# Kernel tuning notes

Hardware: AMD Instinct MI355X
Metric: run time of the kernel (lower is better)

## Reference

```python
import jax, jax.numpy as jnp
import numpy as np

B, N, M, Q, H, D = 1, 512, 512, 128, 8, 16
CLIP = 10.0

def _xavier(key, shape):
    # xavier_uniform over last two dims (fan_in=Q, fan_out=D per head)
    fan_in, fan_out = shape[-2], shape[-1]
    limit = float(np.sqrt(6.0 / (fan_in + fan_out)))
    return jax.random.uniform(key, shape, jnp.float32, -limit, limit)

def setup_inputs() -> dict:
    key = jax.random.key(0)
    ks = jax.random.split(key, 12)
    return {
        "x": jax.random.normal(ks[0], (B, N, Q), jnp.float32),
        "y": jax.random.normal(ks[1], (B, M, Q), jnp.float32),
        "z": jax.random.normal(ks[2], (B, N, M, Q), jnp.float32),
        "mask": jax.random.randint(ks[3], (B, N, M), 0, 2, jnp.int32),
        "lambda_x": _xavier(ks[4], (H, Q, D)),
        "lambda_y": _xavier(ks[5], (H, Q, D)),
        "lambda_z1": _xavier(ks[6], (H, Q, D)),
        "lambda_z2": _xavier(ks[7], (H, Q, D)),
        "bias_lambda_x": jnp.zeros((H, D), jnp.float32),
        "bias_lambda_y": jnp.zeros((H, D), jnp.float32),
        "theta1": _xavier(ks[8], (H, Q, D)),
        "theta2": _xavier(ks[9], (H, Q, D)),
        "bias_theta": jnp.zeros((H, D), jnp.float32),
    }

def reference(x, y, z, mask, lambda_x, lambda_y, lambda_z1, lambda_z2,
              bias_lambda_x, bias_lambda_y, theta1, theta2, bias_theta):
    head_dim = lambda_x.shape[-1]
    # node projections: [B,N,H,D] / [B,M,H,D]
    r_x = jnp.einsum('bnq,hqd->bnhd', x, lambda_x) + bias_lambda_x
    r_y = jnp.einsum('bmq,hqd->bmhd', y, lambda_y) + bias_lambda_y
    # edge projections: [B,N,M,H,D]
    r_z1 = jnp.einsum('bnmq,hqd->bnmhd', z, lambda_z1)
    r_z2 = jnp.einsum('bnmq,hqd->bnmhd', z, lambda_z2)
    # broadcast-add node + edge terms, dot over D -> scores [B,H,N,M]
    att = jnp.einsum('bnmhd,bnmhd->bhnm',
                     r_x[:, :, None, :, :] + r_z1,
                     r_y[:, None, :, :, :] + r_z2)
    att = att * (head_dim ** -0.5)
    att = CLIP * jnp.tanh(att)
    att = jnp.where(mask[:, None, :, :] == 1, -jnp.inf, att)
    # NOTE: softmax over the N (source) axis, matching torch dim=-2
    w = jax.nn.softmax(att, axis=-2)
    x_p = jnp.einsum('bnq,hqd->bnhd', x, theta1)
    r = jnp.einsum('bhnm,bnhd->bmhd', w, x_p) + bias_theta
    return jnp.einsum('bmhd,hqd->bmq', r, theta2)
```

## Files before the change

kernel.cpp:

```cpp
#include <hip/hip_runtime.h>
#include <hip/hip_bf16.h>
#include <math.h>

typedef __attribute__((ext_vector_type(8))) short short8;
typedef __attribute__((ext_vector_type(4))) float f32x4;

__global__ void pack_kernel(const float* __restrict__ lz1,
                            const float* __restrict__ lz2,
                            const float* __restrict__ th2,
                            const float* __restrict__ bth,
                            const float* __restrict__ lx,
                            const float* __restrict__ ly,
                            const float* __restrict__ t1,
                            __hip_bfloat16* __restrict__ Wh,
                            __hip_bfloat16* __restrict__ Wl,
                            float* __restrict__ T2,
                            float* __restrict__ ob,
                            float* __restrict__ Lp) {
    int tid = blockIdx.x * blockDim.x + threadIdx.x;
    int stride = gridDim.x * blockDim.x;
    for (int i = tid; i < 256 * 128; i += stride) {
        int op = i >> 7, q = i & 127;
        int h = op >> 5, wh = (op >> 4) & 1, d = op & 15;
        float v = (wh ? lz2 : lz1)[(h * 128 + q) * 16 + d];
        __hip_bfloat16 hb = __float2bfloat16(v);
        Wh[i] = hb;
        Wl[i] = __float2bfloat16(v - __bfloat162float(hb));
    }
    for (int i = tid; i < 128 * 128; i += stride) {
        int o = i >> 7, q = i & 127;
        int h = o >> 4, d = o & 15;
        T2[i] = th2[(h * 128 + q) * 16 + d];
    }
    for (int i = tid; i < 3 * 128 * 128; i += stride) {
        int which = i >> 14, q = (i >> 7) & 127, o = i & 127;
        int h = o >> 4, d = o & 15;
        const float* S = (which == 0) ? lx : (which == 1) ? ly : t1;
        Lp[i] = S[(h * 128 + q) * 16 + d];
    }
    for (int q = tid; q < 128; q += stride) {
        float s = 0.f;
        for (int h = 0; h < 8; ++h)
            for (int d = 0; d < 16; ++d)
                s += bth[h * 16 + d] * th2[(h * 128 + q) * 16 + d];
        ob[q] = s;
    }
}

__global__ void proj_kernel(const float* __restrict__ x,
                            const float* __restrict__ y,
                            const float* __restrict__ Lp,
                            const float* __restrict__ blx,
                            const float* __restrict__ bly,
                            float* __restrict__ rx,
                            float* __restrict__ ry,
                            float* __restrict__ xp) {
    __shared__ float row[128];
    int n = blockIdx.x;
    int which = blockIdx.y;
    const float* in = (which == 1) ? y : x;
    const float* L  = Lp + which * 16384;
    int o = threadIdx.x;
    row[o] = in[n * 128 + o];
    __syncthreads();
    float a0 = 0.f, a1 = 0.f, a2 = 0.f, a3 = 0.f;
    for (int q = 0; q < 128; q += 4) {
        a0 = fmaf(row[q + 0], L[(q + 0) * 128 + o], a0);
        a1 = fmaf(row[q + 1], L[(q + 1) * 128 + o], a1);
        a2 = fmaf(row[q + 2], L[(q + 2) * 128 + o], a2);
        a3 = fmaf(row[q + 3], L[(q + 3) * 128 + o], a3);
    }
    float acc = (a0 + a1) + (a2 + a3);
    if (which == 0) acc += blx[o];
    if (which == 1) acc += bly[o];
    float* dst = (which == 0) ? rx : (which == 1) ? ry : xp;
    dst[n * 128 + o] = acc;
}

__global__ __launch_bounds__(256) void big_kernel(
        const float* __restrict__ z,
        const int* __restrict__ mask,
        const __hip_bfloat16* __restrict__ Wh,
        const __hip_bfloat16* __restrict__ Wl,
        const float* __restrict__ rx,
        const float* __restrict__ ry,
        float* __restrict__ w) {
    __shared__ short zsh[64 * 128];
    __shared__ short zsl[64 * 128];
    const int m0 = blockIdx.x * 64;
    const int n  = blockIdx.y;
    const int tid = threadIdx.x;

    {
        const int row = tid >> 2, kseg = tid & 3;
        const float* src = &z[((size_t)(n * 512 + m0 + row)) * 128 + kseg * 32];
#pragma unroll
        for (int c8 = 0; c8 < 4; ++c8) {
            float4 v0 = *(const float4*)&src[c8 * 8 + 0];
            float4 v1 = *(const float4*)&src[c8 * 8 + 4];
            float vv[8] = {v0.x, v0.y, v0.z, v0.w, v1.x, v1.y, v1.z, v1.w};
            union { short8 s; __hip_bfloat16 h[8]; } uh, ul;
#pragma unroll
            for (int j = 0; j < 8; ++j) {
                float f = vv[j];
                __hip_bfloat16 hb = __float2bfloat16(f);
                uh.h[j] = hb;
                ul.h[j] = __float2bfloat16(f - __bfloat162float(hb));
            }
            int cw = (kseg * 4 + c8) ^ (row & 7);
            *(short8*)&zsh[row * 128 + cw * 8] = uh.s;
            *(short8*)&zsl[row * 128 + cw * 8] = ul.s;
        }
    }
    __syncthreads();

    const int og = tid >> 6;
    const int l  = tid & 63;
    const int lg = l >> 4;
    const int lm = l & 15;

    const int mk = mask[n * 512 + m0 + l];

#pragma unroll
    for (int p = 0; p < 2; ++p) {
        const int h = og * 2 + p;
        f32x4 acc[4][2];
#pragma unroll
        for (int i = 0; i < 4; ++i) {
            acc[i][0] = (f32x4){0.f, 0.f, 0.f, 0.f};
            acc[i][1] = (f32x4){0.f, 0.f, 0.f, 0.f};
        }

#pragma unroll
        for (int ks = 0; ks < 4; ++ks) {
            short8 bh[2], bl[2];
#pragma unroll
            for (int j = 0; j < 2; ++j) {
                size_t off = (size_t)(og * 64 + (p * 2 + j) * 16 + lm) * 128 + ks * 32 + lg * 8;
                bh[j] = *(const short8*)&Wh[off];
                bl[j] = *(const short8*)&Wl[off];
            }
            short8 ah[4], al[4];
#pragma unroll
            for (int i = 0; i < 4; ++i) {
                int row = i * 16 + lm;
                int cw = (ks * 4 + lg) ^ (row & 7);
                ah[i] = *(const short8*)&zsh[row * 128 + cw * 8];
                al[i] = *(const short8*)&zsl[row * 128 + cw * 8];
            }
#pragma unroll
            for (int i = 0; i < 4; ++i)
#pragma unroll
                for (int j = 0; j < 2; ++j) {
                    acc[i][j] = __builtin_amdgcn_mfma_f32_16x16x32_bf16(bh[j], ah[i], acc[i][j], 0, 0, 0);
                    acc[i][j] = __builtin_amdgcn_mfma_f32_16x16x32_bf16(bh[j], al[i], acc[i][j], 0, 0, 0);
                    acc[i][j] = __builtin_amdgcn_mfma_f32_16x16x32_bf16(bl[j], ah[i], acc[i][j], 0, 0, 0);
                }
        }

        float4 rxt = *(const float4*)&rx[n * 128 + h * 16 + lg * 4];
        const float rxv[4] = {rxt.x, rxt.y, rxt.z, rxt.w};
        float t[4];
#pragma unroll
        for (int i = 0; i < 4; ++i) {
            float4 ryt = *(const float4*)&ry[(size_t)(m0 + i * 16 + lm) * 128 + h * 16 + lg * 4];
            const float ryv[4] = {ryt.x, ryt.y, ryt.z, ryt.w};
            float s = 0.f;
#pragma unroll
            for (int r = 0; r < 4; ++r)
                s = fmaf(rxv[r] + acc[i][0][r], ryv[r] + acc[i][1][r], s);
            s += __shfl_xor(s, 16);
            s += __shfl_xor(s, 32);
            t[i] = s;
        }
        float ta = (lg & 1) ? t[1] : t[0];
        float tb = (lg & 1) ? t[3] : t[2];
        float s  = (lg & 2) ? tb : ta;
        float e1 = __expf(0.5f * s);
        float wv = __expf(-20.f / (e1 + 1.f));
        if (mk == 1) wv = 0.f;
        w[((size_t)(h * 512 + n)) * 512 + m0 + l] = wv;
    }
}

__global__ __launch_bounds__(256) void softpv_kernel(const float* __restrict__ w,
                                                     const float* __restrict__ xp,
                                                     float* __restrict__ rr) {
    __shared__ float xps[512][16];
    __shared__ float red[8][32][16];
    __shared__ float ssum[8][32];
    const int m0 = blockIdx.x * 32;
    const int h  = blockIdx.y;
    const int t  = threadIdx.x;
    const int ml = t & 31, g = t >> 5;

    for (int idx = t; idx < 512 * 4; idx += 256) {
        int nn = idx >> 2, c = idx & 3;
        *(float4*)&xps[nn][c * 4] = *(const float4*)&xp[nn * 128 + h * 16 + c * 4];
    }
    __syncthreads();

    const float* col = &w[((size_t)h * 512) * 512 + m0 + ml];
    float s = 0.f;
    float racc[16];
#pragma unroll
    for (int dd = 0; dd < 16; ++dd) racc[dd] = 0.f;
    for (int nn = g * 64; nn < g * 64 + 64; ++nn) {
        float e = col[(size_t)nn * 512];
        s += e;
#pragma unroll
        for (int c = 0; c < 4; ++c) {
            float4 xv = *(const float4*)&xps[nn][c * 4];
            racc[c * 4 + 0] = fmaf(e, xv.x, racc[c * 4 + 0]);
            racc[c * 4 + 1] = fmaf(e, xv.y, racc[c * 4 + 1]);
            racc[c * 4 + 2] = fmaf(e, xv.z, racc[c * 4 + 2]);
            racc[c * 4 + 3] = fmaf(e, xv.w, racc[c * 4 + 3]);
        }
    }
    ssum[g][ml] = s;
#pragma unroll
    for (int dd = 0; dd < 16; ++dd) red[g][ml][dd] = racc[dd];
    __syncthreads();

    if (t < 128) {
        int ml2 = t & 31, dg = t >> 5;
        float stot = 0.f;
#pragma unroll
        for (int gg = 0; gg < 8; ++gg) stot += ssum[gg][ml2];
        float inv = 1.f / stot;
        float4 o4;
        float* op = (float*)&o4;
#pragma unroll
        for (int j = 0; j < 4; ++j) {
            int dd = dg * 4 + j;
            float v = 0.f;
#pragma unroll
            for (int gg = 0; gg < 8; ++gg) v += red[gg][ml2][dd];
            op[j] = v * inv;
        }
        *(float4*)&rr[(size_t)(m0 + ml2) * 128 + h * 16 + dg * 4] = o4;
    }
}

__global__ void outg_kernel(const float* __restrict__ rr,
                            const float* __restrict__ T2,
                            const float* __restrict__ ob,
                            float* __restrict__ out) {
    __shared__ float rrow[128];
    int m = blockIdx.x;
    int q = threadIdx.x;
    rrow[q] = rr[m * 128 + q];
    __syncthreads();
    float a0 = 0.f, a1 = 0.f, a2 = 0.f, a3 = 0.f;
    for (int o = 0; o < 128; o += 4) {
        a0 = fmaf(rrow[o + 0], T2[(o + 0) * 128 + q], a0);
        a1 = fmaf(rrow[o + 1], T2[(o + 1) * 128 + q], a1);
        a2 = fmaf(rrow[o + 2], T2[(o + 2) * 128 + q], a2);
        a3 = fmaf(rrow[o + 3], T2[(o + 3) * 128 + q], a3);
    }
    out[m * 128 + q] = ob[q] + (a0 + a1) + (a2 + a3);
}

extern "C" void kernel_launch(void* const* d_in, const int* in_sizes, int n_in,
                              void* d_out, int out_size, void* d_ws, size_t ws_size,
                              hipStream_t stream) {
    (void)in_sizes; (void)n_in; (void)out_size; (void)ws_size;
    const float* x   = (const float*)d_in[0];
    const float* y   = (const float*)d_in[1];
    const float* z   = (const float*)d_in[2];
    const int*  mask = (const int*)d_in[3];
    const float* lx  = (const float*)d_in[4];
    const float* ly  = (const float*)d_in[5];
    const float* lz1 = (const float*)d_in[6];
    const float* lz2 = (const float*)d_in[7];
    const float* blx = (const float*)d_in[8];
    const float* bly = (const float*)d_in[9];
    const float* t1  = (const float*)d_in[10];
    const float* t2  = (const float*)d_in[11];
    const float* bth = (const float*)d_in[12];
    float* out = (float*)d_out;

    float* ws = (float*)d_ws;
    float* rx = ws;
    float* ry = rx + 65536;
    float* xp = ry + 65536;
    __hip_bfloat16* Wh = (__hip_bfloat16*)(xp + 65536);
    __hip_bfloat16* Wl = (__hip_bfloat16*)(xp + 65536 + 16384);
    float* T2  = xp + 65536 + 32768;
    float* ob  = T2 + 16384;
    float* Lp  = ob + 128;
    float* wbuf= Lp + 49152;
    float* rr  = wbuf + 2097152;

    pack_kernel<<<dim3(32), dim3(256), 0, stream>>>(lz1, lz2, t2, bth, lx, ly, t1,
                                                    Wh, Wl, T2, ob, Lp);
    proj_kernel<<<dim3(512, 3), dim3(128), 0, stream>>>(x, y, Lp, blx, bly, rx, ry, xp);
    big_kernel<<<dim3(8, 512), dim3(256), 0, stream>>>(z, mask, Wh, Wl, rx, ry, wbuf);
    softpv_kernel<<<dim3(16, 8), dim3(256), 0, stream>>>(wbuf, xp, rr);
    outg_kernel<<<dim3(512), dim3(128), 0, stream>>>(rr, T2, ob, out);
}
```

Measured before the change: 301.9 us.

## Pipeline z loads across n-tiles, hoist weights, retile projection and softmax kernels

The main kernel now handles 8 source rows per block. It double-buffers the bf16 hi/lo split of z in shared memory and prefetches the next z tile into registers while MFMAs run on the current one. The Wh fragments and ry values are hoisted into registers once per block instead of being reloaded for every row. The projection and output kernels each process 4 rows per block to reuse weight loads, and the softpv kernel moves to smaller m tiles with more n-groups for more blocks. The tradeoff is higher register and LDS pressure in the big kernel, and far fewer blocks (512 instead of 4096), which may reduce latency hiding.

```diff
diff --git a/kernel.cpp b/kernel.cpp
--- a/kernel.cpp
+++ b/kernel.cpp
@@ -4,6 +4,8 @@
 
 typedef __attribute__((ext_vector_type(8))) short short8;
 typedef __attribute__((ext_vector_type(4))) float f32x4;
+
+#define NT 8
 
 __global__ void pack_kernel(const float* __restrict__ lz1,
                             const float* __restrict__ lz2,
@@ -38,16 +40,23 @@
         const float* S = (which == 0) ? lx : (which == 1) ? ly : t1;
         Lp[i] = S[(h * 128 + q) * 16 + d];
     }
-    for (int q = tid; q < 128; q += stride) {
+    if (tid < 128) {
+        int q = tid;
         float s = 0.f;
-        for (int h = 0; h < 8; ++h)
-            for (int d = 0; d < 16; ++d)
-                s += bth[h * 16 + d] * th2[(h * 128 + q) * 16 + d];
+#pragma unroll
+        for (int h = 0; h < 8; ++h) {
+#pragma unroll
+            for (int c = 0; c < 4; ++c) {
+                float4 a = *(const float4*)&bth[h * 16 + c * 4];
+                float4 b = *(const float4*)&th2[(h * 128 + q) * 16 + c * 4];
+                s += a.x * b.x + a.y * b.y + a.z * b.z + a.w * b.w;
+            }
+        }
         ob[q] = s;
     }
 }
 
-__global__ void proj_kernel(const float* __restrict__ x,
+__global__ __launch_bounds__(128) void proj_kernel(const float* __restrict__ x,
                             const float* __restrict__ y,
                             const float* __restrict__ Lp,
                             const float* __restrict__ blx,
@@ -55,29 +64,32 @@
                             float* __restrict__ rx,
                             float* __restrict__ ry,
                             float* __restrict__ xp) {
-    __shared__ float row[128];
-    int n = blockIdx.x;
-    int which = blockIdx.y;
+    __shared__ float rows[4][128];
+    const int n0 = blockIdx.x * 4;
+    const int which = blockIdx.y;
     const float* in = (which == 1) ? y : x;
     const float* L  = Lp + which * 16384;
-    int o = threadIdx.x;
-    row[o] = in[n * 128 + o];
-    __syncthreads();
-    float a0 = 0.f, a1 = 0.f, a2 = 0.f, a3 = 0.f;
-    for (int q = 0; q < 128; q += 4) {
-        a0 = fmaf(row[q + 0], L[(q + 0) * 128 + o], a0);
-        a1 = fmaf(row[q + 1], L[(q + 1) * 128 + o], a1);
-        a2 = fmaf(row[q + 2], L[(q + 2) * 128 + o], a2);
-        a3 = fmaf(row[q + 3], L[(q + 3) * 128 + o], a3);
-    }
-    float acc = (a0 + a1) + (a2 + a3);
-    if (which == 0) acc += blx[o];
-    if (which == 1) acc += bly[o];
+    const int o = threadIdx.x;
+#pragma unroll
+    for (int j = 0; j < 4; ++j)
+        rows[j][o] = in[(n0 + j) * 128 + o];
+    __syncthreads();
+    float acc[4] = {0.f, 0.f, 0.f, 0.f};
+#pragma unroll 4
+    for (int q = 0; q < 128; ++q) {
+        float wv = L[q * 128 + o];
+#pragma unroll
+        for (int j = 0; j < 4; ++j)
+            acc[j] = fmaf(rows[j][q], wv, acc[j]);
+    }
+    float b = (which == 0) ? blx[o] : (which == 1) ? bly[o] : 0.f;
     float* dst = (which == 0) ? rx : (which == 1) ? ry : xp;
-    dst[n * 128 + o] = acc;
-}
-
-__global__ __launch_bounds__(256) void big_kernel(
+#pragma unroll
+    for (int j = 0; j < 4; ++j)
+        dst[(n0 + j) * 128 + o] = acc[j] + b;
+}
+
+__global__ __launch_bounds__(256, 2) void big_kernel(
         const float* __restrict__ z,
         const int* __restrict__ mask,
         const __hip_bfloat16* __restrict__ Wh,
@@ -85,114 +97,149 @@
         const float* __restrict__ rx,
         const float* __restrict__ ry,
         float* __restrict__ w) {
-    __shared__ short zsh[64 * 128];
-    __shared__ short zsl[64 * 128];
+    __shared__ short zsh[2][64 * 128];
+    __shared__ short zsl[2][64 * 128];
     const int m0 = blockIdx.x * 64;
-    const int n  = blockIdx.y;
+    const int n0 = blockIdx.y * NT;
     const int tid = threadIdx.x;
-
-    {
-        const int row = tid >> 2, kseg = tid & 3;
-        const float* src = &z[((size_t)(n * 512 + m0 + row)) * 128 + kseg * 32];
-#pragma unroll
-        for (int c8 = 0; c8 < 4; ++c8) {
-            float4 v0 = *(const float4*)&src[c8 * 8 + 0];
-            float4 v1 = *(const float4*)&src[c8 * 8 + 4];
-            float vv[8] = {v0.x, v0.y, v0.z, v0.w, v1.x, v1.y, v1.z, v1.w};
-            union { short8 s; __hip_bfloat16 h[8]; } uh, ul;
-#pragma unroll
-            for (int j = 0; j < 8; ++j) {
-                float f = vv[j];
-                __hip_bfloat16 hb = __float2bfloat16(f);
-                uh.h[j] = hb;
-                ul.h[j] = __float2bfloat16(f - __bfloat162float(hb));
-            }
-            int cw = (kseg * 4 + c8) ^ (row & 7);
-            *(short8*)&zsh[row * 128 + cw * 8] = uh.s;
-            *(short8*)&zsl[row * 128 + cw * 8] = ul.s;
-        }
-    }
-    __syncthreads();
-
     const int og = tid >> 6;
     const int l  = tid & 63;
     const int lg = l >> 4;
     const int lm = l & 15;
 
-    const int mk = mask[n * 512 + m0 + l];
-
-#pragma unroll
-    for (int p = 0; p < 2; ++p) {
-        const int h = og * 2 + p;
-        f32x4 acc[4][2];
-#pragma unroll
-        for (int i = 0; i < 4; ++i) {
-            acc[i][0] = (f32x4){0.f, 0.f, 0.f, 0.f};
-            acc[i][1] = (f32x4){0.f, 0.f, 0.f, 0.f};
+    const int srow = tid >> 2, kseg = tid & 3;
+    const float* zbase = &z[(size_t)(m0 + srow) * 128 + kseg * 32];
+
+    short8 bhr[2][4][2];
+#pragma unroll
+    for (int p = 0; p < 2; ++p)
+#pragma unroll
+        for (int ks = 0; ks < 4; ++ks)
+#pragma unroll
+            for (int j = 0; j < 2; ++j)
+                bhr[p][ks][j] = *(const short8*)&Wh[(size_t)(og * 64 + (p * 2 + j) * 16 + lm) * 128 + ks * 32 + lg * 8];
+
+    float4 ryr[2][4];
+#pragma unroll
+    for (int p = 0; p < 2; ++p)
+#pragma unroll
+        for (int i = 0; i < 4; ++i)
+            ryr[p][i] = *(const float4*)&ry[(size_t)(m0 + i * 16 + lm) * 128 + (og * 2 + p) * 16 + lg * 4];
+
+    float4 zr[8];
+#define LOADZ(nn)                                                         \
+    {                                                                     \
+        const float* p_ = zbase + (size_t)(nn) * 65536;                   \
+        _Pragma("unroll")                                                 \
+        for (int c_ = 0; c_ < 8; ++c_) zr[c_] = *(const float4*)&p_[c_ * 4]; \
+    }
+
+#define CONVERT_WRITE(b)                                                  \
+    {                                                                     \
+        _Pragma("unroll")                                                 \
+        for (int c8 = 0; c8 < 4; ++c8) {                                  \
+            float vv[8] = {zr[2 * c8].x, zr[2 * c8].y, zr[2 * c8].z, zr[2 * c8].w, \
+                           zr[2 * c8 + 1].x, zr[2 * c8 + 1].y, zr[2 * c8 + 1].z, zr[2 * c8 + 1].w}; \
+            union { short8 s; __hip_bfloat16 h[8]; } uh, ul;              \
+            _Pragma("unroll")                                             \
+            for (int jj = 0; jj < 8; ++jj) {                              \
+                float f_ = vv[jj];                                        \
+                __hip_bfloat16 hb_ = __float2bfloat16(f_);                \
+                uh.h[jj] = hb_;                                           \
+                ul.h[jj] = __float2bfloat16(f_ - __bfloat162float(hb_));  \
+            }                                                             \
+            int cw_ = (kseg * 4 + c8) ^ (srow & 7);                       \
+            *(short8*)&zsh[b][srow * 128 + cw_ * 8] = uh.s;               \
+            *(short8*)&zsl[b][srow * 128 + cw_ * 8] = ul.s;               \
+        }                                                                 \
+    }
+
+    LOADZ(n0);
+    CONVERT_WRITE(0);
+    LOADZ(n0 + 1);
+    __syncthreads();
+
+    for (int t = 0; t < NT; ++t) {
+        const int n = n0 + t;
+        const int cur = t & 1;
+        const int mk = mask[n * 512 + m0 + l];
+
+#pragma unroll
+        for (int p = 0; p < 2; ++p) {
+            const int h = og * 2 + p;
+            f32x4 acc[4][2];
+#pragma unroll
+            for (int i = 0; i < 4; ++i) {
+                acc[i][0] = (f32x4){0.f, 0.f, 0.f, 0.f};
+                acc[i][1] = (f32x4){0.f, 0.f, 0.f, 0.f};
+            }
+#pragma unroll
+            for (int ks = 0; ks < 4; ++ks) {
+                short8 bl[2];
+#pragma unroll
+                for (int j = 0; j < 2; ++j)
+                    bl[j] = *(const short8*)&Wl[(size_t)(og * 64 + (p * 2 + j) * 16 + lm) * 128 + ks * 32 + lg * 8];
+                short8 ah[4], al[4];
+#pragma unroll
+                for (int i = 0; i < 4; ++i) {
+                    int row = i * 16 + lm;
+                    int cw = (ks * 4 + lg) ^ (row & 7);
+                    ah[i] = *(const short8*)&zsh[cur][row * 128 + cw * 8];
+                    al[i] = *(const short8*)&zsl[cur][row * 128 + cw * 8];
+                }
+#pragma unroll
+                for (int i = 0; i < 4; ++i)
+#pragma unroll
+                    for (int j = 0; j < 2; ++j) {
+                        acc[i][j] = __builtin_amdgcn_mfma_f32_16x16x32_bf16(bhr[p][ks][j], ah[i], acc[i][j], 0, 0, 0);
+                        acc[i][j] = __builtin_amdgcn_mfma_f32_16x16x32_bf16(bhr[p][ks][j], al[i], acc[i][j], 0, 0, 0);
+                        acc[i][j] = __builtin_amdgcn_mfma_f32_16x16x32_bf16(bl[j], ah[i], acc[i][j], 0, 0, 0);
+                    }
+            }
+
+            float4 rxt = *(const float4*)&rx[n * 128 + h * 16 + lg * 4];
+            const float rxv[4] = {rxt.x, rxt.y, rxt.z, rxt.w};
+            float t4[4];
+#pragma unroll
+            for (int i = 0; i < 4; ++i) {
+                const float ryv[4] = {ryr[p][i].x, ryr[p][i].y, ryr[p][i].z, ryr[p][i].w};
+                float s = 0.f;
+#pragma unroll
+                for (int r = 0; r < 4; ++r)
+                    s = fmaf(rxv[r] + acc[i][0][r], ryv[r] + acc[i][1][r], s);
+                s += __shfl_xor(s, 16);
+                s += __shfl_xor(s, 32);
+                t4[i] = s;
+            }
+            float ta = (lg & 1) ? t4[1] : t4[0];
+            float tb = (lg & 1) ? t4[3] : t4[2];
+            float s  = (lg & 2) ? tb : ta;
+            float e1 = __expf(0.5f * s);
+            float wv = __expf(-20.f / (e1 + 1.f));
+            if (mk == 1) wv = 0.f;
+            w[((size_t)(h * 512 + n)) * 512 + m0 + l] = wv;
         }
 
-#pragma unroll
-        for (int ks = 0; ks < 4; ++ks) {
-            short8 bh[2], bl[2];
-#pragma unroll
-            for (int j = 0; j < 2; ++j) {
-                size_t off = (size_t)(og * 64 + (p * 2 + j) * 16 + lm) * 128 + ks * 32 + lg * 8;
-                bh[j] = *(const short8*)&Wh[off];
-                bl[j] = *(const short8*)&Wl[off];
-            }
-            short8 ah[4], al[4];
-#pragma unroll
-            for (int i = 0; i < 4; ++i) {
-                int row = i * 16 + lm;
-                int cw = (ks * 4 + lg) ^ (row & 7);
-                ah[i] = *(const short8*)&zsh[row * 128 + cw * 8];
-                al[i] = *(const short8*)&zsl[row * 128 + cw * 8];
-            }
-#pragma unroll
-            for (int i = 0; i < 4; ++i)
-#pragma unroll
-                for (int j = 0; j < 2; ++j) {
-                    acc[i][j] = __builtin_amdgcn_mfma_f32_16x16x32_bf16(bh[j], ah[i], acc[i][j], 0, 0, 0);
-                    acc[i][j] = __builtin_amdgcn_mfma_f32_16x16x32_bf16(bh[j], al[i], acc[i][j], 0, 0, 0);
-                    acc[i][j] = __builtin_amdgcn_mfma_f32_16x16x32_bf16(bl[j], ah[i], acc[i][j], 0, 0, 0);
-                }
+        if (t + 1 < NT) {
+            CONVERT_WRITE(cur ^ 1);
+            if (t + 2 < NT) LOADZ(n0 + t + 2);
         }
-
-        float4 rxt = *(const float4*)&rx[n * 128 + h * 16 + lg * 4];
-        const float rxv[4] = {rxt.x, rxt.y, rxt.z, rxt.w};
-        float t[4];
-#pragma unroll
-        for (int i = 0; i < 4; ++i) {
-            float4 ryt = *(const float4*)&ry[(size_t)(m0 + i * 16 + lm) * 128 + h * 16 + lg * 4];
-            const float ryv[4] = {ryt.x, ryt.y, ryt.z, ryt.w};
-            float s = 0.f;
-#pragma unroll
-            for (int r = 0; r < 4; ++r)
-                s = fmaf(rxv[r] + acc[i][0][r], ryv[r] + acc[i][1][r], s);
-            s += __shfl_xor(s, 16);
-            s += __shfl_xor(s, 32);
-            t[i] = s;
-        }
-        float ta = (lg & 1) ? t[1] : t[0];
-        float tb = (lg & 1) ? t[3] : t[2];
-        float s  = (lg & 2) ? tb : ta;
-        float e1 = __expf(0.5f * s);
-        float wv = __expf(-20.f / (e1 + 1.f));
-        if (mk == 1) wv = 0.f;
-        w[((size_t)(h * 512 + n)) * 512 + m0 + l] = wv;
-    }
+        __syncthreads();
+    }
+#undef LOADZ
+#undef CONVERT_WRITE
 }
 
 __global__ __launch_bounds__(256) void softpv_kernel(const float* __restrict__ w,
                                                      const float* __restrict__ xp,
                                                      float* __restrict__ rr) {
     __shared__ float xps[512][16];
-    __shared__ float red[8][32][16];
-    __shared__ float ssum[8][32];
-    const int m0 = blockIdx.x * 32;
+    __shared__ float red[16][16][16];
+    __shared__ float ssum[16][16];
+    const int m0 = blockIdx.x * 16;
     const int h  = blockIdx.y;
     const int t  = threadIdx.x;
-    const int ml = t & 31, g = t >> 5;
+    const int ml = t & 15, g = t >> 4;
 
     for (int idx = t; idx < 512 * 4; idx += 256) {
         int nn = idx >> 2, c = idx & 3;
@@ -205,7 +252,7 @@
     float racc[16];
 #pragma unroll
     for (int dd = 0; dd < 16; ++dd) racc[dd] = 0.f;
-    for (int nn = g * 64; nn < g * 64 + 64; ++nn) {
+    for (int nn = g * 32; nn < g * 32 + 32; ++nn) {
         float e = col[(size_t)nn * 512];
         s += e;
 #pragma unroll
@@ -222,43 +269,41 @@
     for (int dd = 0; dd < 16; ++dd) red[g][ml][dd] = racc[dd];
     __syncthreads();
 
-    if (t < 128) {
-        int ml2 = t & 31, dg = t >> 5;
+    {
+        const int m = t & 15, dd = t >> 4;
         float stot = 0.f;
 #pragma unroll
-        for (int gg = 0; gg < 8; ++gg) stot += ssum[gg][ml2];
-        float inv = 1.f / stot;
-        float4 o4;
-        float* op = (float*)&o4;
-#pragma unroll
-        for (int j = 0; j < 4; ++j) {
-            int dd = dg * 4 + j;
-            float v = 0.f;
-#pragma unroll
-            for (int gg = 0; gg < 8; ++gg) v += red[gg][ml2][dd];
-            op[j] = v * inv;
-        }
-        *(float4*)&rr[(size_t)(m0 + ml2) * 128 + h * 16 + dg * 4] = o4;
-    }
-}
-
-__global__ void outg_kernel(const float* __restrict__ rr,
+        for (int gg = 0; gg < 16; ++gg) stot += ssum[gg][m];
+        float v = 0.f;
+#pragma unroll
+        for (int gg = 0; gg < 16; ++gg) v += red[gg][m][dd];
+        rr[(size_t)(m0 + m) * 128 + h * 16 + dd] = v / stot;
+    }
+}
+
+__global__ __launch_bounds__(128) void outg_kernel(const float* __restrict__ rr,
                             const float* __restrict__ T2,
                             const float* __restrict__ ob,
                             float* __restrict__ out) {
-    __shared__ float rrow[128];
-    int m = blockIdx.x;
-    int q = threadIdx.x;
-    rrow[q] = rr[m * 128 + q];
-    __syncthreads();
-    float a0 = 0.f, a1 = 0.f, a2 = 0.f, a3 = 0.f;
-    for (int o = 0; o < 128; o += 4) {
-        a0 = fmaf(rrow[o + 0], T2[(o + 0) * 128 + q], a0);
-        a1 = fmaf(rrow[o + 1], T2[(o + 1) * 128 + q], a1);
-        a2 = fmaf(rrow[o + 2], T2[(o + 2) * 128 + q], a2);
-        a3 = fmaf(rrow[o + 3], T2[(o + 3) * 128 + q], a3);
-    }
-    out[m * 128 + q] = ob[q] + (a0 + a1) + (a2 + a3);
+    __shared__ float rrow[4][128];
+    const int m0 = blockIdx.x * 4;
+    const int q = threadIdx.x;
+#pragma unroll
+    for (int j = 0; j < 4; ++j)
+        rrow[j][q] = rr[(m0 + j) * 128 + q];
+    __syncthreads();
+    float acc[4] = {0.f, 0.f, 0.f, 0.f};
+#pragma unroll 4
+    for (int o = 0; o < 128; ++o) {
+        float tv = T2[o * 128 + q];
+#pragma unroll
+        for (int j = 0; j < 4; ++j)
+            acc[j] = fmaf(rrow[j][o], tv, acc[j]);
+    }
+    float b = ob[q];
+#pragma unroll
+    for (int j = 0; j < 4; ++j)
+        out[(m0 + j) * 128 + q] = acc[j] + b;
 }
 
 extern "C" void kernel_launch(void* const* d_in, const int* in_sizes, int n_in,
@@ -294,8 +339,8 @@
 
     pack_kernel<<<dim3(32), dim3(256), 0, stream>>>(lz1, lz2, t2, bth, lx, ly, t1,
                                                     Wh, Wl, T2, ob, Lp);
-    proj_kernel<<<dim3(512, 3), dim3(128), 0, stream>>>(x, y, Lp, blx, bly, rx, ry, xp);
-    big_kernel<<<dim3(8, 512), dim3(256), 0, stream>>>(z, mask, Wh, Wl, rx, ry, wbuf);
-    softpv_kernel<<<dim3(16, 8), dim3(256), 0, stream>>>(wbuf, xp, rr);
-    outg_kernel<<<dim3(512), dim3(128), 0, stream>>>(rr, T2, ob, out);
-}
+    proj_kernel<<<dim3(128, 3), dim3(128), 0, stream>>>(x, y, Lp, blx, bly, rx, ry, xp);
+    big_kernel<<<dim3(8, 64), dim3(256), 0, stream>>>(z, mask, Wh, Wl, rx, ry, wbuf);
+    softpv_kernel<<<dim3(32, 8), dim3(256), 0, stream>>>(wbuf, xp, rr);
+    outg_kernel<<<dim3(128), dim3(128), 0, stream>>>(rr, T2, ob, out);
+}
```

New measurement: 303.7 us. Within noise of the previous version (+0.6%).
